# Kernel optimization log

Measured on AMD Instinct MI355X. Metric: run time of the kernel, lower is better.

The kernel has to match this reference:

```python
import jax, jax.numpy as jnp
import numpy as np

HIDDEN_DIM = 768
N_HEAD = 12
ATTN_DIM = HIDDEN_DIM // N_HEAD  # 64
SCALE = jnp.sqrt(jnp.float32(ATTN_DIM))


def setup_inputs() -> dict:
    key = jax.random.key(0)
    ks = jax.random.split(key, 6)
    B, S = 8, 2048
    return {
        "query": jax.random.normal(ks[0], (B, S, HIDDEN_DIM), dtype=jnp.float32),
        "key": jax.random.normal(ks[1], (B, S, HIDDEN_DIM), dtype=jnp.float32),
        "value": jax.random.normal(ks[2], (B, S, HIDDEN_DIM), dtype=jnp.float32),
        "Wq": jax.random.normal(ks[3], (ATTN_DIM, HIDDEN_DIM), dtype=jnp.float32) * 0.02,
        "Wk": jax.random.normal(ks[4], (ATTN_DIM, HIDDEN_DIM), dtype=jnp.float32) * 0.02,
        "Wv": jax.random.normal(ks[5], (ATTN_DIM, HIDDEN_DIM), dtype=jnp.float32) * 0.02,
    }


def reference(query, key, value, Wq, Wk, Wv):
    # Linear projections (bias=False): x @ W.T -> [B, S, attn_dim]
    q = jnp.einsum("bsh,dh->bsd", query, Wq)
    k = jnp.einsum("bsh,dh->bsd", key, Wk)
    v = jnp.einsum("bsh,dh->bsd", value, Wv)
    # Scaled dot-product scores: [B, S, S]
    scores = jnp.einsum("bqd,bkd->bqk", q, k) / SCALE
    attn = jax.nn.softmax(scores, axis=-1)  # dropout p=0 -> identity in eval
    # Weighted sum of values: [B, S, attn_dim]
    return jnp.einsum("bqk,bkd->bqd", attn, v)
```

## Files before the change

kernel.cpp:

```cpp
#include <hip/hip_runtime.h>

typedef short s16x8 __attribute__((ext_vector_type(8)));
typedef float f32x4 __attribute__((ext_vector_type(4)));
typedef unsigned short us4 __attribute__((ext_vector_type(4)));

static __device__ __forceinline__ unsigned short f2bf(float f) {
  unsigned u = __builtin_bit_cast(unsigned, f);
  u += 0x7FFFu + ((u >> 16) & 1u);
  return (unsigned short)(u >> 16);
}

#define MFMA16(a, b, c) __builtin_amdgcn_mfma_f32_16x16x32_bf16((a), (b), (c), 0, 0, 0)

__global__ __launch_bounds__(256) void proj_kernel(
    const float* __restrict__ Xq, const float* __restrict__ Xk, const float* __restrict__ Xv,
    const float* __restrict__ Wq, const float* __restrict__ Wk, const float* __restrict__ Wv,
    unsigned short* __restrict__ qf,
    unsigned short* __restrict__ kf,
    unsigned short* __restrict__ vfo)
{
  __shared__ __align__(16) unsigned short xs[64][72];
  __shared__ __align__(16) unsigned short ws[64][72];

  const int bid = blockIdx.x;
  const int t = bid >> 8;
  const int rb = bid & 255;
  const int b = rb >> 5;
  const int stile = rb & 31;
  const float* X = (t == 0) ? Xq : (t == 1) ? Xk : Xv;
  const float* W = (t == 0) ? Wq : (t == 1) ? Wk : Wv;

  const int tid = threadIdx.x;
  const int wv = tid >> 6;
  const int lane = tid & 63;
  const int j = lane & 15;
  const int g = lane >> 4;

  f32x4 acc[4];
#pragma unroll
  for (int i = 0; i < 4; ++i) acc[i] = {0.f, 0.f, 0.f, 0.f};

  const size_t xrow0 = (size_t)b * 2048 + (size_t)stile * 64;

  for (int kc = 0; kc < 768; kc += 64) {
#pragma unroll
    for (int p = 0; p < 4; ++p) {
      int lin = p * 256 + tid;
      int row = lin >> 4;
      int seg = lin & 15;
      float4 xv = *(const float4*)(X + (xrow0 + row) * 768 + kc + seg * 4);
      us4 px; px.x = f2bf(xv.x); px.y = f2bf(xv.y); px.z = f2bf(xv.z); px.w = f2bf(xv.w);
      *(us4*)&xs[row][seg * 4] = px;
      float4 wv4 = *(const float4*)(W + (size_t)row * 768 + kc + seg * 4);
      us4 pw; pw.x = f2bf(wv4.x); pw.y = f2bf(wv4.y); pw.z = f2bf(wv4.z); pw.w = f2bf(wv4.w);
      *(us4*)&ws[row][seg * 4] = pw;
    }
    __syncthreads();
    s16x8 a0 = *(const s16x8*)&xs[wv * 16 + j][g * 8];
    s16x8 a1 = *(const s16x8*)&xs[wv * 16 + j][32 + g * 8];
#pragma unroll
    for (int ct = 0; ct < 4; ++ct) {
      s16x8 b0 = *(const s16x8*)&ws[ct * 16 + j][g * 8];
      s16x8 b1 = *(const s16x8*)&ws[ct * 16 + j][32 + g * 8];
      acc[ct] = MFMA16(a0, b0, acc[ct]);
      acc[ct] = MFMA16(a1, b1, acc[ct]);
    }
    __syncthreads();
  }

  unsigned short* fb = &xs[0][0];
  if (t < 2) {
    const float sc = (t == 0) ? 0.125f : 1.0f;
#pragma unroll
    for (int ct = 0; ct < 4; ++ct) {
      int base16 = wv * 1024 + ((ct >= 2) ? 512 : 0) + (((ct & 1) * 2 + (j >> 3)) * 128) + (j & 7);
#pragma unroll
      for (int r = 0; r < 4; ++r)
        fb[base16 + (g * 4 + r) * 8] = f2bf(acc[ct][r] * sc);
    }
    __syncthreads();
    unsigned short* dst = ((t == 0) ? qf : kf) + ((size_t)b * 128 + stile * 4) * 1024;
#pragma unroll
    for (int p2 = 0; p2 < 2; ++p2) {
      int idx = p2 * 2048 + tid * 8;
      *(s16x8*)(dst + idx) = *(const s16x8*)&fb[idx];
    }
  } else {
#pragma unroll
    for (int ct = 0; ct < 4; ++ct) {
      us4 pk;
      pk.x = f2bf(acc[ct][0]); pk.y = f2bf(acc[ct][1]);
      pk.z = f2bf(acc[ct][2]); pk.w = f2bf(acc[ct][3]);
      *(us4*)&fb[ct * 1024 + ((wv >= 2) ? 512 : 0) +
                 (((wv & 1) * 2 + (g >> 1)) * 16 + j) * 8 + (g & 1) * 4] = pk;
    }
    __syncthreads();
    unsigned short* gb = vfo + ((size_t)b * 32 + stile) * 4096;
#pragma unroll
    for (int p2 = 0; p2 < 2; ++p2) {
      int idx = p2 * 2048 + tid * 8;
      *(s16x8*)(gb + idx) = *(const s16x8*)&fb[idx];
    }
  }
}

__global__ __launch_bounds__(512, 4) void attn_kernel(
    const unsigned short* __restrict__ qf,
    const unsigned short* __restrict__ kf,
    const unsigned short* __restrict__ vf,
    float* __restrict__ out)
{
  __shared__ __align__(16) unsigned char raw[69632];
  __shared__ float lls[8][32];
  unsigned short* p_lds = (unsigned short*)raw;
  float* comb = (float*)raw;

  const int tid = threadIdx.x;
  const int wv = tid >> 6;
  const int lane = tid & 63;
  const int j = lane & 15;
  const int g = lane >> 4;
  const int sg = wv >> 2;
  const int c = wv & 3;

  const int bid0 = blockIdx.x;
  const int swz = (bid0 & 7) * 32 + (bid0 >> 3);
  const int b = swz >> 5;
  const int qt = swz & 31;

  s16x8 q0[2], q1[2];
#pragma unroll
  for (int rg = 0; rg < 2; ++rg) {
    const unsigned short* qp =
        qf + ((size_t)(b * 128 + qt * 4 + sg * 2 + rg)) * 1024 + lane * 8;
    q0[rg] = *(const s16x8*)(qp);
    q1[rg] = *(const s16x8*)(qp + 512);
  }

  f32x4 o[2][4];
#pragma unroll
  for (int rg = 0; rg < 2; ++rg)
#pragma unroll
    for (int i = 0; i < 4; ++i) o[rg][i] = {0.f, 0.f, 0.f, 0.f};
  float l_acc[2] = {0.f, 0.f};

  const unsigned short* kfb = kf + (size_t)b * 131072 + c * 32768 + lane * 8;
  const unsigned short* vfb = vf + (size_t)b * 131072 + c * 32768 + lane * 8;
  unsigned short* myp0 = p_lds + (size_t)((wv * 2 + 0) * 16 + j) * 72;
  unsigned short* myp1 = p_lds + (size_t)((wv * 2 + 1) * 16 + j) * 72;

  for (int kt = 0; kt < 8; ++kt) {
    const unsigned short* kc_ = kfb + kt * 4096;
    s16x8 ka[4], kb2[4];
#pragma unroll
    for (int ct = 0; ct < 4; ++ct) {
      ka[ct] = *(const s16x8*)(kc_ + ct * 1024);
      kb2[ct] = *(const s16x8*)(kc_ + ct * 1024 + 512);
    }
    {
      f32x4 st[4];
#pragma unroll
      for (int ct = 0; ct < 4; ++ct) {
        f32x4 z = {0.f, 0.f, 0.f, 0.f};
        z = MFMA16(ka[ct], q0[0], z);
        z = MFMA16(kb2[ct], q1[0], z);
        st[ct] = z;
      }
#pragma unroll
      for (int ct = 0; ct < 4; ++ct) {
        float p0 = __expf(st[ct][0]);
        float p1 = __expf(st[ct][1]);
        float p2 = __expf(st[ct][2]);
        float p3 = __expf(st[ct][3]);
        l_acc[0] += (p0 + p1) + (p2 + p3);
        us4 pk; pk.x = f2bf(p0); pk.y = f2bf(p1); pk.z = f2bf(p2); pk.w = f2bf(p3);
        *(us4*)&myp0[ct * 16 + g * 4] = pk;
      }
    }
    {
      f32x4 st[4];
#pragma unroll
      for (int ct = 0; ct < 4; ++ct) {
        f32x4 z = {0.f, 0.f, 0.f, 0.f};
        z = MFMA16(ka[ct], q0[1], z);
        z = MFMA16(kb2[ct], q1[1], z);
        st[ct] = z;
      }
#pragma unroll
      for (int ct = 0; ct < 4; ++ct) {
        float p0 = __expf(st[ct][0]);
        float p1 = __expf(st[ct][1]);
        float p2 = __expf(st[ct][2]);
        float p3 = __expf(st[ct][3]);
        l_acc[1] += (p0 + p1) + (p2 + p3);
        us4 pk; pk.x = f2bf(p0); pk.y = f2bf(p1); pk.z = f2bf(p2); pk.w = f2bf(p3);
        *(us4*)&myp1[ct * 16 + g * 4] = pk;
      }
    }
    const unsigned short* vc_ = vfb + kt * 4096;
    s16x8 va[4], vb2[4];
#pragma unroll
    for (int dt = 0; dt < 4; ++dt) {
      va[dt] = *(const s16x8*)(vc_ + dt * 1024);
      vb2[dt] = *(const s16x8*)(vc_ + dt * 1024 + 512);
    }
    s16x8 pa0 = *(const s16x8*)&myp0[g * 8];
    s16x8 pa1 = *(const s16x8*)&myp0[32 + g * 8];
#pragma unroll
    for (int dt = 0; dt < 4; ++dt) {
      o[0][dt] = MFMA16(pa0, va[dt], o[0][dt]);
      o[0][dt] = MFMA16(pa1, vb2[dt], o[0][dt]);
    }
    s16x8 pb0 = *(const s16x8*)&myp1[g * 8];
    s16x8 pb1 = *(const s16x8*)&myp1[32 + g * 8];
#pragma unroll
    for (int dt = 0; dt < 4; ++dt) {
      o[1][dt] = MFMA16(pb0, va[dt], o[1][dt]);
      o[1][dt] = MFMA16(pb1, vb2[dt], o[1][dt]);
    }
  }

#pragma unroll
  for (int rg = 0; rg < 2; ++rg) {
    l_acc[rg] += __shfl_xor(l_acc[rg], 16);
    l_acc[rg] += __shfl_xor(l_acc[rg], 32);
  }

  __syncthreads();
#pragma unroll
  for (int rg = 0; rg < 2; ++rg) {
#pragma unroll
    for (int dt = 0; dt < 4; ++dt)
#pragma unroll
      for (int r = 0; r < 4; ++r)
        comb[((size_t)wv * 32 + rg * 16 + g * 4 + r) * 68 + dt * 16 + j] = o[rg][dt][r];
    if (g == 0) lls[wv][rg * 16 + j] = l_acc[rg];
  }
  __syncthreads();

#pragma unroll
  for (int it = 0; it < 8; ++it) {
    const int idx = it * 512 + tid;
    const int row = idx >> 6;
    const int d = idx & 63;
    const int ssg = row >> 5;
    const int srow = row & 31;
    float s = 0.f, lt = 0.f;
#pragma unroll
    for (int cc = 0; cc < 4; ++cc) {
      s += comb[((size_t)(ssg * 4 + cc) * 32 + srow) * 68 + d];
      lt += lls[ssg * 4 + cc][srow];
    }
    out[(((size_t)b * 2048) + qt * 64 + row) * 64 + d] = s / lt;
  }
}

extern "C" void kernel_launch(void* const* d_in, const int* in_sizes, int n_in,
                              void* d_out, int out_size, void* d_ws, size_t ws_size,
                              hipStream_t stream) {
  const float* query = (const float*)d_in[0];
  const float* key_  = (const float*)d_in[1];
  const float* value = (const float*)d_in[2];
  const float* Wq = (const float*)d_in[3];
  const float* Wk = (const float*)d_in[4];
  const float* Wv = (const float*)d_in[5];

  unsigned short* qfb = (unsigned short*)d_ws;
  unsigned short* kfb = qfb + 1048576u;
  unsigned short* vfb = qfb + 2u * 1048576u;
  float* outp = (float*)d_out;

  hipLaunchKernelGGL(proj_kernel, dim3(768), dim3(256), 0, stream,
                     query, key_, value, Wq, Wk, Wv, qfb, kfb, vfb);
  hipLaunchKernelGGL(attn_kernel, dim3(256), dim3(512), 0, stream,
                     qfb, kfb, vfb, outp);
}
```

Before: 47.93 us.

## Fold log2e into Q scale, use exp2, packed bf16 cvt, hoist V loads, setprio

Folds log2(e) into the Q projection scale so the softmax can use the hardware exp2 directly. Replaces the manual bf16 rounding with the packed v_cvt_pk_bf16_f32 instruction. Moves the V tile global loads ahead of the QK MFMAs so they overlap with compute, and wraps the MFMA sections in s_setprio. Also widens the P LDS row stride from 72 to 136, which uses more LDS and may need a matching allocation in the part of the code not shown.

```diff
diff --git a/kernel.cpp b/kernel.cpp
--- a/kernel.cpp
+++ b/kernel.cpp
@@ -9,6 +9,20 @@
   u += 0x7FFFu + ((u >> 16) & 1u);
   return (unsigned short)(u >> 16);
 }
+
+static __device__ __forceinline__ unsigned cvtpk(float lo, float hi) {
+  unsigned r;
+  asm("v_cvt_pk_bf16_f32 %0, %1, %2" : "=v"(r) : "v"(lo), "v"(hi));
+  return r;
+}
+
+#if __has_builtin(__builtin_amdgcn_exp2f)
+#define EXP2(x) __builtin_amdgcn_exp2f(x)
+#else
+#define EXP2(x) __expf((x) * 0.69314718056f)
+#endif
+
+#define QSCALE 0.1803368801111204f
 
 #define MFMA16(a, b, c) __builtin_amdgcn_mfma_f32_16x16x32_bf16((a), (b), (c), 0, 0, 0)
 
@@ -70,7 +84,7 @@
 
   unsigned short* fb = &xs[0][0];
   if (t < 2) {
-    const float sc = (t == 0) ? 0.125f : 1.0f;
+    const float sc = (t == 0) ? QSCALE : 1.0f;
 #pragma unroll
     for (int ct = 0; ct < 4; ++ct) {
       int base16 = wv * 1024 + ((ct >= 2) ? 512 : 0) + (((ct & 1) * 2 + (j >> 3)) * 128) + (j & 7);
@@ -146,19 +160,26 @@
 
   const unsigned short* kfb = kf + (size_t)b * 131072 + c * 32768 + lane * 8;
   const unsigned short* vfb = vf + (size_t)b * 131072 + c * 32768 + lane * 8;
-  unsigned short* myp0 = p_lds + (size_t)((wv * 2 + 0) * 16 + j) * 72;
-  unsigned short* myp1 = p_lds + (size_t)((wv * 2 + 1) * 16 + j) * 72;
+  unsigned short* myp0 = p_lds + (size_t)((wv * 2 + 0) * 16 + j) * 136;
+  unsigned short* myp1 = p_lds + (size_t)((wv * 2 + 1) * 16 + j) * 136;
 
   for (int kt = 0; kt < 8; ++kt) {
     const unsigned short* kc_ = kfb + kt * 4096;
-    s16x8 ka[4], kb2[4];
+    const unsigned short* vc_ = vfb + kt * 4096;
+    s16x8 ka[4], kb2[4], va[4], vb2[4];
 #pragma unroll
     for (int ct = 0; ct < 4; ++ct) {
       ka[ct] = *(const s16x8*)(kc_ + ct * 1024);
       kb2[ct] = *(const s16x8*)(kc_ + ct * 1024 + 512);
     }
+#pragma unroll
+    for (int dt = 0; dt < 4; ++dt) {
+      va[dt] = *(const s16x8*)(vc_ + dt * 1024);
+      vb2[dt] = *(const s16x8*)(vc_ + dt * 1024 + 512);
+    }
     {
       f32x4 st[4];
+      __builtin_amdgcn_s_setprio(1);
 #pragma unroll
       for (int ct = 0; ct < 4; ++ct) {
         f32x4 z = {0.f, 0.f, 0.f, 0.f};
@@ -166,19 +187,21 @@
         z = MFMA16(kb2[ct], q1[0], z);
         st[ct] = z;
       }
-#pragma unroll
-      for (int ct = 0; ct < 4; ++ct) {
-        float p0 = __expf(st[ct][0]);
-        float p1 = __expf(st[ct][1]);
-        float p2 = __expf(st[ct][2]);
-        float p3 = __expf(st[ct][3]);
+      __builtin_amdgcn_s_setprio(0);
+#pragma unroll
+      for (int ct = 0; ct < 4; ++ct) {
+        float p0 = EXP2(st[ct][0]);
+        float p1 = EXP2(st[ct][1]);
+        float p2 = EXP2(st[ct][2]);
+        float p3 = EXP2(st[ct][3]);
         l_acc[0] += (p0 + p1) + (p2 + p3);
-        us4 pk; pk.x = f2bf(p0); pk.y = f2bf(p1); pk.z = f2bf(p2); pk.w = f2bf(p3);
-        *(us4*)&myp0[ct * 16 + g * 4] = pk;
+        uint2 u; u.x = cvtpk(p0, p1); u.y = cvtpk(p2, p3);
+        *(uint2*)&myp0[ct * 16 + g * 4] = u;
       }
     }
     {
       f32x4 st[4];
+      __builtin_amdgcn_s_setprio(1);
 #pragma unroll
       for (int ct = 0; ct < 4; ++ct) {
         f32x4 z = {0.f, 0.f, 0.f, 0.f};
@@ -186,38 +209,34 @@
         z = MFMA16(kb2[ct], q1[1], z);
         st[ct] = z;
       }
-#pragma unroll
-      for (int ct = 0; ct < 4; ++ct) {
-        float p0 = __expf(st[ct][0]);
-        float p1 = __expf(st[ct][1]);
-        float p2 = __expf(st[ct][2]);
-        float p3 = __expf(st[ct][3]);
+      __builtin_amdgcn_s_setprio(0);
+#pragma unroll
+      for (int ct = 0; ct < 4; ++ct) {
+        float p0 = EXP2(st[ct][0]);
+        float p1 = EXP2(st[ct][1]);
+        float p2 = EXP2(st[ct][2]);
+        float p3 = EXP2(st[ct][3]);
         l_acc[1] += (p0 + p1) + (p2 + p3);
-        us4 pk; pk.x = f2bf(p0); pk.y = f2bf(p1); pk.z = f2bf(p2); pk.w = f2bf(p3);
-        *(us4*)&myp1[ct * 16 + g * 4] = pk;
-      }
-    }
-    const unsigned short* vc_ = vfb + kt * 4096;
-    s16x8 va[4], vb2[4];
-#pragma unroll
-    for (int dt = 0; dt < 4; ++dt) {
-      va[dt] = *(const s16x8*)(vc_ + dt * 1024);
-      vb2[dt] = *(const s16x8*)(vc_ + dt * 1024 + 512);
+        uint2 u; u.x = cvtpk(p0, p1); u.y = cvtpk(p2, p3);
+        *(uint2*)&myp1[ct * 16 + g * 4] = u;
+      }
     }
     s16x8 pa0 = *(const s16x8*)&myp0[g * 8];
     s16x8 pa1 = *(const s16x8*)&myp0[32 + g * 8];
+    s16x8 pb0 = *(const s16x8*)&myp1[g * 8];
+    s16x8 pb1 = *(const s16x8*)&myp1[32 + g * 8];
+    __builtin_amdgcn_s_setprio(1);
 #pragma unroll
     for (int dt = 0; dt < 4; ++dt) {
       o[0][dt] = MFMA16(pa0, va[dt], o[0][dt]);
       o[0][dt] = MFMA16(pa1, vb2[dt], o[0][dt]);
     }
-    s16x8 pb0 = *(const s16x8*)&myp1[g * 8];
-    s16x8 pb1 = *(const s16x8*)&myp1[32 + g * 8];
 #pragma unroll
     for (int dt = 0; dt < 4; ++dt) {
       o[1][dt] = MFMA16(pb0, va[dt], o[1][dt]);
       o[1][dt] = MFMA16(pb1, vb2[dt], o[1][dt]);
     }
+    __builtin_amdgcn_s_setprio(0);
   }
 
 #pragma unroll
```

After: 54.43 us. +13.5%, slower.
